# Optimization experiments

Measured on AMD Instinct MI355X. Metric: run time of the kernel, lower is better.

Reference implementation:

```python
import jax, jax.numpy as jnp
from jax import lax
import numpy as np

B, T, N, HORIZON = 64, 12, 512, 12
IN_DIM = 1; OUT_DIM = 1; YCOV = 1
RNN = 64; MEM_NUM = 20; MEM_DIM = 64; EMB = 10; CHEB_K = 3
DEC_DIM = RNN + MEM_DIM  # 128


def _xavier(key, shape):
    fan_in, fan_out = shape[0], shape[-1]
    std = float(np.sqrt(2.0 / (fan_in + fan_out)))
    return jax.random.normal(key, shape, dtype=jnp.float32) * std


def _cheb_feats(A, x, batched):
    mm = (lambda a, v: jnp.einsum('bnm,bmc->bnc', a, v)) if batched else (lambda a, v: jnp.einsum('nm,bmc->bnc', a, v))
    gs = [x, mm(A, x)]
    for _ in range(CHEB_K - 2):
        gs.append(2.0 * mm(A, gs[-1]) - gs[-2])
    return jnp.concatenate(gs, axis=-1)


def _agcn(x, A, W, b, batched):
    return _cheb_feats(A, x, batched) @ W + b


def _cell(x, state, A, Wg, bg, Wu, bu, batched):
    # AGCRN GRU cell
    hid = state.shape[-1]
    inp = jnp.concatenate([x, state], axis=-1)
    z_r = jax.nn.sigmoid(_agcn(inp, A, Wg, bg, batched))
    z, r = z_r[..., :hid], z_r[..., hid:]
    cand = jnp.concatenate([x, z * state], axis=-1)
    hc = jnp.tanh(_agcn(cand, A, Wu, bu, batched))
    return r * state + (1.0 - r) * hc


def _encode(x, A, Wg, bg, Wu, bu):
    # x: [B,T,N,C] -> last hidden state [B,N,RNN]
    xt = jnp.swapaxes(x, 0, 1)  # [T,B,N,C]
    init = jnp.zeros((x.shape[0], x.shape[2], RNN), x.dtype)
    def step(state, xt_):
        h = _cell(xt_, state, A, Wg, bg, Wu, bu, batched=False)
        return h, None
    h_t, _ = lax.scan(step, init, xt)
    return h_t


def _query_memory(h_t, Memory, Wq):
    q = h_t @ Wq                                   # [B,N,mem_dim]
    att = jax.nn.softmax(q @ Memory.T, axis=-1)    # [B,N,mem_num]
    value = att @ Memory                           # [B,N,mem_dim]
    _, ind = lax.top_k(att, 2)
    pos = Memory[ind[..., 0]]                      # [B,N,mem_dim]
    return value, pos


def setup_inputs() -> dict:
    key = jax.random.key(0)
    ks = jax.random.split(key, 20)
    x = jax.random.normal(ks[0], (B, T, N, IN_DIM), dtype=jnp.float32)
    x_cov = jax.random.normal(ks[1], (B, T, N, 1), dtype=jnp.float32)
    x_his = jax.random.normal(ks[2], (B, T, N, IN_DIM), dtype=jnp.float32)
    y_cov = jax.random.normal(ks[3], (B, HORIZON, N, YCOV), dtype=jnp.float32)
    a = jax.random.uniform(ks[4], (N, N), dtype=jnp.float32)
    adj = a / jnp.sum(a, axis=-1, keepdims=True)
    enc_in = IN_DIM + RNN
    dec_in = OUT_DIM + YCOV + DEC_DIM
    return {
        'x': x, 'x_cov': x_cov, 'x_his': x_his, 'y_cov': y_cov, 'adj': adj,
        'enc_gate_W': _xavier(ks[5], (CHEB_K * enc_in, 2 * RNN)),
        'enc_gate_b': jnp.zeros((2 * RNN,), jnp.float32),
        'enc_upd_W': _xavier(ks[6], (CHEB_K * enc_in, RNN)),
        'enc_upd_b': jnp.zeros((RNN,), jnp.float32),
        'dec_gate_W': _xavier(ks[7], (CHEB_K * dec_in, 2 * DEC_DIM)),
        'dec_gate_b': jnp.zeros((2 * DEC_DIM,), jnp.float32),
        'dec_upd_W': _xavier(ks[8], (CHEB_K * dec_in, DEC_DIM)),
        'dec_upd_b': jnp.zeros((DEC_DIM,), jnp.float32),
        'Memory': _xavier(ks[9], (MEM_NUM, MEM_DIM)),
        'Wq': _xavier(ks[10], (RNN, MEM_DIM)),
        'hyper_W': _xavier(ks[11], (DEC_DIM, EMB)),
        'hyper_b': jnp.zeros((EMB,), jnp.float32),
        'lat_W': _xavier(ks[12], (MEM_DIM, 1)),
        'lat_b': jnp.zeros((1,), jnp.float32),
        'proj_W': _xavier(ks[13], (DEC_DIM, OUT_DIM)),
        'proj_b': jnp.zeros((OUT_DIM,), jnp.float32),
    }


def reference(x, x_cov, x_his, y_cov, adj,
              enc_gate_W, enc_gate_b, enc_upd_W, enc_upd_b,
              dec_gate_W, dec_gate_b, dec_upd_W, dec_upd_b,
              Memory, Wq, hyper_W, hyper_b, lat_W, lat_b, proj_W, proj_b):
    # --- encoder on x and x_his (shared weights, single static support) ---
    h_t = _encode(x, adj, enc_gate_W, enc_gate_b, enc_upd_W, enc_upd_b)
    h_att, pos = _query_memory(h_t, Memory, Wq)
    h_his_t = _encode(x_his, adj, enc_gate_W, enc_gate_b, enc_upd_W, enc_upd_b)
    _, pos_his = _query_memory(h_his_t, Memory, Wq)
    # schema==1 latent distance head (sigmoid activation)
    latent_dis = jax.nn.sigmoid(((pos - pos_his) @ lat_W + lat_b)[..., 0])  # [B,N]
    # --- adaptive decoder support from hypernetwork ---
    h_aug = jnp.concatenate([h_t, h_att], axis=-1)          # [B,N,DEC_DIM]
    node_emb = h_aug @ hyper_W + hyper_b                    # [B,N,EMB]
    support = jax.nn.softmax(jax.nn.relu(jnp.einsum('bnc,bmc->bnm', node_emb, node_emb)), axis=-1)  # [B,N,N]
    # --- decoder rollout (inference path, no teacher forcing) ---
    go0 = jnp.zeros((x.shape[0], N, OUT_DIM), x.dtype)
    ycov_t = jnp.swapaxes(y_cov, 0, 1)  # [HORIZON,B,N,YCOV]
    def dec_step(carry, yc):
        go, h = carry
        xt = jnp.concatenate([go, yc], axis=-1)
        h = _cell(xt, h, support, dec_gate_W, dec_gate_b, dec_upd_W, dec_upd_b, batched=True)
        go = h @ proj_W + proj_b
        return (go, h), go
    _, outs = lax.scan(dec_step, (go0, h_aug), ycov_t)
    output = jnp.swapaxes(outs, 0, 1)  # [B,HORIZON,N,OUT_DIM]
    return output, latent_dis
```

## Files before the change

kernel.cpp:

```cpp
#include <hip/hip_runtime.h>
#include <hip/hip_bf16.h>


typedef __attribute__((ext_vector_type(8))) short s8v;
typedef __attribute__((ext_vector_type(4))) float f4v;
typedef __attribute__((ext_vector_type(4))) unsigned short u4v;

__device__ __forceinline__ float b2f(unsigned short u){
  union{unsigned int i; float f;} v; v.i = ((unsigned int)u)<<16; return v.f;
}
__device__ __forceinline__ unsigned short f2b(float f){
  union{float f; unsigned int i;} v; v.f = f;
  unsigned int r = v.i + 0x7fff + ((v.i >> 16) & 1);
  return (unsigned short)(r >> 16);
}

__global__ void k_zero16(uint4* p, int n){
  int i = blockIdx.x*256 + threadIdx.x;
  if (i < n) p[i] = make_uint4(0,0,0,0);
}


__global__ void k_reorderF(const float* __restrict__ W, float* __restrict__ Wr,
                           int HC, int NEX, int SEGW, int J){
  int idx = blockIdx.x*256 + threadIdx.x;
  int K = 3*SEGW;
  if (idx >= K*J) return;
  int k = idx / J, j = idx - k*J;
  int seg = k / SEGW, c = k - seg*SEGW;
  int CIN = HC + NEX;
  float v = 0.f;
  if (c < HC)       v = W[(size_t)(seg*CIN + NEX + c)*J + j];
  else if (c < CIN) v = W[(size_t)(seg*CIN + (c-HC))*J + j];
  Wr[(size_t)k*J + j] = v;
}

__global__ __launch_bounds__(256) void k_a2e(const float* __restrict__ A,
                                             float* __restrict__ A2e){
  __shared__ __align__(16) float As[32][132];
  __shared__ __align__(16) float Bs[32][132];
  int t = threadIdx.x;
  int r0 = (blockIdx.x & 3) * 128;
  int c0 = (blockIdx.x >> 2) * 128;
  int tr = t & 15, tc = t >> 4;
  float acc[8][8];
  #pragma unroll
  for (int i=0;i<8;i++)
    #pragma unroll
    for (int j=0;j<8;j++) acc[i][j]=0.f;
  for (int k0=0;k0<512;k0+=32){
    #pragma unroll
    for (int i=0;i<4;i++){
      int s = t + i*256;
      int k = s & 31, rq = s >> 5;
      const float* ap = A + (size_t)(r0 + rq*4)*512 + k0 + k;
      float4 v;
      v.x = ap[0]; v.y = ap[512]; v.z = ap[1024]; v.w = ap[1536];
      *(float4*)&As[k][rq*4] = v;
    }
    #pragma unroll
    for (int i=0;i<4;i++){
      int s = t + i*256;
      int k = s >> 5, cq = s & 31;
      float4 v = *(const float4*)(A + (size_t)(k0+k)*512 + c0 + cq*4);
      *(float4*)&Bs[k][cq*4] = v;
    }
    __syncthreads();
    #pragma unroll 8
    for (int k=0;k<32;k++){
      float a[8], b[8];
      *(float4*)&a[0] = *(const float4*)&As[k][tr*4];
      *(float4*)&a[4] = *(const float4*)&As[k][64+tr*4];
      *(float4*)&b[0] = *(const float4*)&Bs[k][tc*4];
      *(float4*)&b[4] = *(const float4*)&Bs[k][64+tc*4];
      #pragma unroll
      for (int i=0;i<8;i++)
        #pragma unroll
        for (int j=0;j<8;j++) acc[i][j] += a[i]*b[j];
    }
    __syncthreads();
  }
  #pragma unroll
  for (int i=0;i<8;i++){
    int r = r0 + (i<4 ? tr*4+i : 64+tr*4+i-4);
    #pragma unroll
    for (int j=0;j<8;j++){
      int c = c0 + (j<4 ? tc*4+j : 64+tc*4+j-4);
      A2e[(size_t)r*512 + c] = 2.f*acc[i][j] - (r==c ? 1.f : 0.f);
    }
  }
}

__global__ __launch_bounds__(256) void k_mm2F(
    const float* __restrict__ A, const float* __restrict__ A2e,
    const float* __restrict__ hsrc,
    const float* __restrict__ xa, const float* __restrict__ xb,
    int tstep, float* __restrict__ feats)
{
  __shared__ __align__(16) float As[32][68];
  __shared__ __align__(16) float A2s[32][68];
  __shared__ __align__(16) float Bs0[32][68];
  __shared__ __align__(16) float Bs1[32][68];
  const int t = threadIdx.x;
  const int z = blockIdx.z;
  const int n0 = blockIdx.x * 64;
  const int tr = t & 15, tc = t >> 4;
  const int xrow = t & 63, xmat = (t >> 6) & 1, xbb = t >> 7;
  const float* xp0 = xa + ((size_t)z*12 + tstep)*512;
  const float* xp1 = xb + ((size_t)z*12 + tstep)*512;
  float acc[2][2][4][4];
  #pragma unroll
  for (int m=0;m<2;m++)
    #pragma unroll
    for (int b=0;b<2;b++)
      #pragma unroll
      for (int i=0;i<4;i++)
        #pragma unroll
        for (int j=0;j<4;j++) acc[m][b][i][j]=0.f;
  float xacc = 0.f;

  for (int k0=0;k0<512;k0+=32){
    #pragma unroll
    for (int i=0;i<2;i++){
      int s = t + i*256;
      int k = s & 31, rq = s >> 5;
      const float* ap  = A   + (size_t)(n0 + rq*4)*512 + k0 + k;
      const float* a2p = A2e + (size_t)(n0 + rq*4)*512 + k0 + k;
      float4 v, w;
      v.x = ap[0];  v.y = ap[512];  v.z = ap[1024];  v.w = ap[1536];
      w.x = a2p[0]; w.y = a2p[512]; w.z = a2p[1024]; w.w = a2p[1536];
      *(float4*)&As[k][rq*4]  = v;
      *(float4*)&A2s[k][rq*4] = w;
    }
    #pragma unroll
    for (int i=0;i<2;i++){
      int s = t + i*256;
      int k = s >> 4, cq = s & 15;
      *(float4*)&Bs0[k][cq*4] = *(const float4*)(hsrc + (size_t)(z*512 + k0 + k)*64 + cq*4);
      *(float4*)&Bs1[k][cq*4] = *(const float4*)(hsrc + (size_t)((z+64)*512 + k0 + k)*64 + cq*4);
    }
    if (t < 32)      Bs0[t][64]    = xp0[k0 + t];
    else if (t < 64) Bs1[t-32][64] = xp1[k0 + t - 32];
    __syncthreads();
    #pragma unroll 4
    for (int k=0;k<32;k++){
      float a1[4], a2[4], b0[4], b1[4];
      *(float4*)&a1[0] = *(const float4*)&As[k][tr*4];
      *(float4*)&a2[0] = *(const float4*)&A2s[k][tr*4];
      *(float4*)&b0[0] = *(const float4*)&Bs0[k][tc*4];
      *(float4*)&b1[0] = *(const float4*)&Bs1[k][tc*4];
      #pragma unroll
      for (int i=0;i<4;i++)
        #pragma unroll
        for (int j=0;j<4;j++){
          acc[0][0][i][j] += a1[i]*b0[j];
          acc[0][1][i][j] += a1[i]*b1[j];
          acc[1][0][i][j] += a2[i]*b0[j];
          acc[1][1][i][j] += a2[i]*b1[j];
        }
      float am = xmat ? A2s[k][xrow] : As[k][xrow];
      xacc += am * (xbb ? Bs1[k][64] : Bs0[k][64]);
    }
    if ((k0 >> 6) == (int)blockIdx.x){
      for (int s=t; s<1088; s+=256){
        int sb = (s >= 544) ? 1 : 0;
        int ss = s - sb*544;
        int kk = ss/17, q = ss - kk*17;
        int bb = z + sb*64;
        float4 v;
        if (q < 16) v = sb ? *(const float4*)&Bs1[kk][q*4] : *(const float4*)&Bs0[kk][q*4];
        else        v = make_float4(sb ? Bs1[kk][64] : Bs0[kk][64], 0.f, 0.f, 0.f);
        *(float4*)(feats + (size_t)(bb*512 + k0 + kk)*204 + q*4) = v;
      }
    }
    __syncthreads();
  }
  #pragma unroll
  for (int bbi=0;bbi<2;bbi++){
    const int bb = z + bbi*64;
    #pragma unroll
    for (int i=0;i<4;i++){
      int row = n0 + tr*4 + i;
      float* fr = feats + (size_t)(bb*512 + row)*204;
      float4 v;
      v.x=acc[0][bbi][i][0]; v.y=acc[0][bbi][i][1];
      v.z=acc[0][bbi][i][2]; v.w=acc[0][bbi][i][3];
      *(float4*)(fr + 68 + tc*4) = v;
      v.x=acc[1][bbi][i][0]; v.y=acc[1][bbi][i][1];
      v.z=acc[1][bbi][i][2]; v.w=acc[1][bbi][i][3];
      *(float4*)(fr + 136 + tc*4) = v;
    }
  }
  feats[(size_t)((z + xbb*64)*512 + n0 + xrow)*204 + (xmat ? 136 : 68) + 64] = xacc;
}

__global__ __launch_bounds__(256) void k_gwG(
    const float* __restrict__ feats, const float* __restrict__ Wr,
    const float* __restrict__ bias,
    const float* __restrict__ hbuf, float* __restrict__ zh, float* __restrict__ rbuf)
{
  __shared__ __align__(16) float As[17][132];
  __shared__ __align__(16) float Ws[17][132];
  const int t = threadIdx.x;
  const int row0 = blockIdx.x * 128;
  const int tr = t & 15, tc = t >> 4;
  float acc[2][2][4][4];
  #pragma unroll
  for (int rg=0;rg<2;rg++)
    #pragma unroll
    for (int cg=0;cg<2;cg++)
      #pragma unroll
      for (int i=0;i<4;i++)
        #pragma unroll
        for (int j=0;j<4;j++) acc[rg][cg][i][j]=0.f;
  for (int kc=0; kc<204; kc+=17){
    for (int s=t; s<2176; s+=256){
      int r = s/17, k = s - r*17;
      As[k][r] = feats[(size_t)(row0+r)*204 + kc + k];
    }
    for (int s=t; s<2176; s+=256){
      int k = s >> 7, j = s & 127;
      Ws[k][j] = Wr[(size_t)(kc+k)*128 + j];
    }
    __syncthreads();
    #pragma unroll
    for (int k=0;k<17;k++){
      float a[8], w[8];
      *(float4*)&a[0] = *(const float4*)&As[k][tr*4];
      *(float4*)&a[4] = *(const float4*)&As[k][64+tr*4];
      *(float4*)&w[0] = *(const float4*)&Ws[k][tc*4];
      *(float4*)&w[4] = *(const float4*)&Ws[k][64+tc*4];
      #pragma unroll
      for (int rg=0;rg<2;rg++)
        #pragma unroll
        for (int i=0;i<4;i++)
          #pragma unroll
          for (int cg=0;cg<2;cg++)
            #pragma unroll
            for (int j=0;j<4;j++)
              acc[rg][cg][i][j] += a[rg*4+i]*w[cg*4+j];
    }
    __syncthreads();
  }
  float bj0[4], bj1[4];
  #pragma unroll
  for (int j=0;j<4;j++){ bj0[j] = bias[tc*4+j]; bj1[j] = bias[64+tc*4+j]; }
  #pragma unroll
  for (int rg=0;rg<2;rg++){
    #pragma unroll
    for (int i=0;i<4;i++){
      int row = row0 + rg*64 + tr*4 + i;
      float4 h4 = *(const float4*)(hbuf + (size_t)row*64 + tc*4);
      float hv[4] = {h4.x,h4.y,h4.z,h4.w};
      float4 oz, orr;
      float z[4], rr[4];
      #pragma unroll
      for (int j=0;j<4;j++){
        z[j]  = 1.f/(1.f + __expf(-(acc[rg][0][i][j] + bj0[j])));
        rr[j] = 1.f/(1.f + __expf(-(acc[rg][1][i][j] + bj1[j])));
      }
      oz.x=z[0]*hv[0]; oz.y=z[1]*hv[1]; oz.z=z[2]*hv[2]; oz.w=z[3]*hv[3];
      orr.x=rr[0]; orr.y=rr[1]; orr.z=rr[2]; orr.w=rr[3];
      *(float4*)(zh   + (size_t)row*64 + tc*4) = oz;
      *(float4*)(rbuf + (size_t)row*64 + tc*4) = orr;
    }
  }
}

__global__ __launch_bounds__(256) void k_gwU(
    const float* __restrict__ feats, const float* __restrict__ Wr,
    const float* __restrict__ bias,
    float* __restrict__ henc, const float* __restrict__ rbuf)
{
  __shared__ __align__(16) float As[17][132];
  __shared__ __align__(16) float Ws[17][68];
  const int t = threadIdx.x;
  const int row0 = blockIdx.x * 128;
  const int tr = t & 15, tc = t >> 4;
  float acc[2][4][4];
  #pragma unroll
  for (int rg=0;rg<2;rg++)
    #pragma unroll
    for (int i=0;i<4;i++)
      #pragma unroll
      for (int j=0;j<4;j++) acc[rg][i][j]=0.f;
  for (int kc=0; kc<204; kc+=17){
    for (int s=t; s<2176; s+=256){
      int r = s/17, k = s - r*17;
      As[k][r] = feats[(size_t)(row0+r)*204 + kc + k];
    }
    for (int s=t; s<1088; s+=256){
      int k = s >> 6, j = s & 63;
      Ws[k][j] = Wr[(size_t)(kc+k)*64 + j];
    }
    __syncthreads();
    #pragma unroll
    for (int k=0;k<17;k++){
      float a[8], w[4];
      *(float4*)&a[0] = *(const float4*)&As[k][tr*4];
      *(float4*)&a[4] = *(const float4*)&As[k][64+tr*4];
      *(float4*)&w[0] = *(const float4*)&Ws[k][tc*4];
      #pragma unroll
      for (int rg=0;rg<2;rg++)
        #pragma unroll
        for (int i=0;i<4;i++)
          #pragma unroll
          for (int j=0;j<4;j++)
            acc[rg][i][j] += a[rg*4+i]*w[j];
    }
    __syncthreads();
  }
  float bj[4];
  #pragma unroll
  for (int j=0;j<4;j++) bj[j] = bias[tc*4+j];
  #pragma unroll
  for (int rg=0;rg<2;rg++){
    #pragma unroll
    for (int i=0;i<4;i++){
      int row = row0 + rg*64 + tr*4 + i;
      float4 h4 = *(const float4*)(henc + (size_t)row*64 + tc*4);
      float4 r4 = *(const float4*)(rbuf + (size_t)row*64 + tc*4);
      float hv[4] = {h4.x,h4.y,h4.z,h4.w};
      float rv[4] = {r4.x,r4.y,r4.z,r4.w};
      float ov[4];
      #pragma unroll
      for (int j=0;j<4;j++){
        float hc = 1.f - 2.f/(__expf(2.f*(acc[rg][i][j] + bj[j])) + 1.f);
        ov[j] = rv[j]*hv[j] + (1.f - rv[j])*hc;
      }
      float4 o; o.x=ov[0]; o.y=ov[1]; o.z=ov[2]; o.w=ov[3];
      *(float4*)(henc + (size_t)row*64 + tc*4) = o;
    }
  }
}


__global__ void k_reorderB(const float* __restrict__ W, unsigned short* __restrict__ Wr,
                           int HC, int NEX, int C, int KP, int J){
  int idx = blockIdx.x*256 + threadIdx.x;
  if (idx >= J*KP) return;
  int j = idx / KP, kp = idx - j*KP;
  float v = 0.f;
  if (kp < 3*C){
    int seg = kp / C, c = kp - seg*C;
    int CIN = HC + NEX;
    if (c < HC)       v = W[(size_t)(seg*CIN + NEX + c)*J + j];
    else if (c < CIN) v = W[(size_t)(seg*CIN + (c-HC))*J + j];
  }
  Wr[(size_t)j*KP + kp] = f2b(v);
}

template<int C16, bool BETA>
__global__ __launch_bounds__(256) void k_mmB(
    const unsigned short* __restrict__ M, long long mstride,
    unsigned short* fC, int C3, int xseg, int oseg,
    unsigned short* fR, int KP, float alpha)
{
  constexpr int C = C16*16;
  constexpr int BIT = (C*4 + 255)/256;
  __shared__ unsigned short Bs[C*40];
  const int t = threadIdx.x;
  const int w = t >> 6, L = t & 63, lm = L & 15, q = L >> 4;
  const int bb = blockIdx.z;
  const int n0 = blockIdx.x * 128;
  const unsigned short* Mb = M + (size_t)bb * mstride;
  unsigned short* fCb = fC + (size_t)bb * C3 * 512;
  const unsigned short* Xb = fCb + (size_t)xseg * C * 512;
  const unsigned short* Yb = fCb;
  unsigned short* Ob = fCb + (size_t)oseg * C * 512;
  const int rw = n0 + w*32;

  f4v acc[2][C16];
  #pragma unroll
  for (int i=0;i<2;i++)
    #pragma unroll
    for (int j=0;j<C16;j++)
      #pragma unroll
      for (int r=0;r<4;r++) acc[i][j][r] = 0.f;

  s8v breg[BIT];
  const size_t ar0 = (size_t)(rw + lm)*512 + q*8;
  const size_t ar1 = (size_t)(rw + 16 + lm)*512 + q*8;

  #pragma unroll
  for (int i=0;i<BIT;i++){
    int s = t + i*256;
    if (s < C*4) breg[i] = *(const s8v*)(Xb + (size_t)(s>>2)*512 + (s&3)*8);
  }
  s8v a0 = *(const s8v*)(Mb + ar0);
  s8v a1 = *(const s8v*)(Mb + ar1);

  for (int ks=0; ks<16; ks++){
    #pragma unroll
    for (int i=0;i<BIT;i++){
      int s = t + i*256;
      if (s < C*4) *(s8v*)&Bs[(s>>2)*40 + (s&3)*8] = breg[i];
    }
    __syncthreads();
    const int kn = (ks < 15) ? (ks+1)*32 : 0;
    #pragma unroll
    for (int i=0;i<BIT;i++){
      int s = t + i*256;
      if (s < C*4) breg[i] = *(const s8v*)(Xb + (size_t)(s>>2)*512 + kn + (s&3)*8);
    }
    s8v a0n = *(const s8v*)(Mb + ar0 + kn);
    s8v a1n = *(const s8v*)(Mb + ar1 + kn);
    #pragma unroll
    for (int ct=0; ct<C16; ct++){
      s8v b = *(const s8v*)&Bs[(ct*16+lm)*40 + q*8];
      acc[0][ct] = __builtin_amdgcn_mfma_f32_16x16x32_bf16(a0, b, acc[0][ct], 0,0,0);
      acc[1][ct] = __builtin_amdgcn_mfma_f32_16x16x32_bf16(a1, b, acc[1][ct], 0,0,0);
    }
    __syncthreads();
    a0 = a0n; a1 = a1n;
  }
  #pragma unroll
  for (int rt=0; rt<2; rt++){
    const int m0 = rw + rt*16 + q*4;
    #pragma unroll
    for (int ct=0; ct<C16; ct++){
      const int c = ct*16 + lm;
      u4v o;
      if (BETA){
        u4v y = *(const u4v*)(Yb + (size_t)c*512 + m0);
        #pragma unroll
        for (int r=0;r<4;r++) o[r] = f2b(alpha*acc[rt][ct][r] - b2f(y[r]));
      } else {
        #pragma unroll
        for (int r=0;r<4;r++) o[r] = f2b(acc[rt][ct][r]);
      }
      *(u4v*)(Ob + (size_t)c*512 + m0) = o;
      const size_t rbase = (size_t)(bb*512 + m0)*KP + oseg*C + c;
      #pragma unroll
      for (int r=0;r<4;r++) fR[rbase + (size_t)r*KP] = o[r];
    }
  }
}

template<int KSTEPS, int JT16, int MODE, int HC>
__global__ __launch_bounds__(256) void k_gwB(
    unsigned short* fR, int KP,
    const unsigned short* __restrict__ Wr, const float* __restrict__ bias,
    unsigned short* fC, int C3,
    float* hC, float* rbuf)
{
  constexpr int JT = JT16*16;
  constexpr int BIT = JT*4/256;
  __shared__ unsigned short Bs[JT*40];
  const int t = threadIdx.x;
  const int w = t >> 6, L = t & 63, lm = L & 15, q = L >> 4;
  const int row0 = blockIdx.x * 128;
  const int j0 = blockIdx.y * JT;
  const int rw = row0 + w*32;

  f4v acc[2][JT16];
  #pragma unroll
  for (int i=0;i<2;i++)
    #pragma unroll
    for (int j=0;j<JT16;j++)
      #pragma unroll
      for (int r=0;r<4;r++) acc[i][j][r] = 0.f;

  s8v breg[BIT];
  const unsigned short* Wb = Wr + (size_t)j0*KP;
  const size_t ar0 = (size_t)(rw + lm)*KP + q*8;
  const size_t ar1 = (size_t)(rw + 16 + lm)*KP + q*8;

  #pragma unroll
  for (int i=0;i<BIT;i++){
    int s = t + i*256;
    breg[i] = *(const s8v*)(Wb + (size_t)(s>>2)*KP + (s&3)*8);
  }
  s8v a0 = *(const s8v*)(fR + ar0);
  s8v a1 = *(const s8v*)(fR + ar1);

  for (int ks=0; ks<KSTEPS; ks++){
    #pragma unroll
    for (int i=0;i<BIT;i++){
      int s = t + i*256;
      *(s8v*)&Bs[(s>>2)*40 + (s&3)*8] = breg[i];
    }
    __syncthreads();
    const int kn = (ks < KSTEPS-1) ? (ks+1)*32 : 0;
    #pragma unroll
    for (int i=0;i<BIT;i++){
      int s = t + i*256;
      breg[i] = *(const s8v*)(Wb + (size_t)(s>>2)*KP + kn + (s&3)*8);
    }
    s8v a0n = *(const s8v*)(fR + ar0 + kn);
    s8v a1n = *(const s8v*)(fR + ar1 + kn);
    #pragma unroll
    for (int ct=0; ct<JT16; ct++){
      s8v b = *(const s8v*)&Bs[(ct*16+lm)*40 + q*8];
      acc[0][ct] = __builtin_amdgcn_mfma_f32_16x16x32_bf16(a0, b, acc[0][ct], 0,0,0);
      acc[1][ct] = __builtin_amdgcn_mfma_f32_16x16x32_bf16(a1, b, acc[1][ct], 0,0,0);
    }
    __syncthreads();
    a0 = a0n; a1 = a1n;
  }
  #pragma unroll
  for (int rt=0; rt<2; rt++){
    const int m0 = rw + rt*16 + q*4;
    const int bb = m0 >> 9, n = m0 & 511;
    #pragma unroll
    for (int ct=0; ct<JT16; ct++){
      const int j = j0 + ct*16 + lm;
      const float bj = bias[j];
      if (MODE == 0){
        if (j < HC){
          f4v h4 = *(const f4v*)(hC + ((size_t)bb*HC + j)*512 + n);
          u4v o;
          #pragma unroll
          for (int r=0;r<4;r++){
            float s = 1.f/(1.f + __expf(-(acc[rt][ct][r] + bj)));
            float zh = s * h4[r];
            o[r] = f2b(zh);
            fR[(size_t)(m0+r)*KP + j] = o[r];
          }
          *(u4v*)(fC + ((size_t)bb*C3 + j)*512 + n) = o;
        } else {
          f4v rv;
          #pragma unroll
          for (int r=0;r<4;r++) rv[r] = 1.f/(1.f + __expf(-(acc[rt][ct][r] + bj)));
          *(f4v*)(rbuf + ((size_t)bb*HC + (j-HC))*512 + n) = rv;
        }
      } else {
        f4v h4 = *(const f4v*)(hC + ((size_t)bb*HC + j)*512 + n);
        f4v r4 = *(const f4v*)(rbuf + ((size_t)bb*HC + j)*512 + n);
        u4v o; f4v hn;
        #pragma unroll
        for (int r=0;r<4;r++){
          float e = __expf(2.f*(acc[rt][ct][r] + bj));
          float hc_ = 1.f - 2.f/(e + 1.f);
          hn[r] = r4[r]*h4[r] + (1.f - r4[r])*hc_;
          o[r] = f2b(hn[r]);
          fR[(size_t)(m0+r)*KP + j] = o[r];
        }
        *(f4v*)(hC + ((size_t)bb*HC + j)*512 + n) = hn;
        *(u4v*)(fC + ((size_t)bb*C3 + j)*512 + n) = o;
      }
    }
  }
}


__global__ void k_extras_dec(const float* __restrict__ yc,
    unsigned short* fR, unsigned short* fC, int tstep){
  int rr = blockIdx.x*256 + threadIdx.x;
  int bb = rr >> 9, n = rr & 511;
  unsigned short u = f2b(yc[((size_t)bb*12 + tstep)*512 + n]);
  fR[(size_t)rr*448 + 129] = u;
  fC[((size_t)bb*432 + 129)*512 + n] = u;
}
__global__ void k_fix_go(unsigned short* fR, unsigned short* fC){
  int rr = blockIdx.x*256 + threadIdx.x;
  int bb = rr >> 9, n = rr & 511;
  fR[(size_t)rr*448 + 128] = 0;
  fC[((size_t)bb*432 + 128)*512 + n] = 0;
}

__global__ __launch_bounds__(256) void k_query(const float* __restrict__ hR,
      const float* __restrict__ Wq, const float* __restrict__ Mem,
      float* __restrict__ hCd, unsigned short* fR, unsigned short* fC,
      int* __restrict__ it, int* __restrict__ ih){
  int sub = threadIdx.x >> 6, lane = threadIdx.x & 63;
  int row = blockIdx.x*4 + sub;
  __shared__ float sh[4][64], sq[4][64], ss[4][20];
  float hv = hR[(size_t)row*64 + lane];
  sh[sub][lane] = hv;
  __syncthreads();
  float qv = 0.f;
  for (int c=0;c<64;c++) qv += sh[sub][c]*Wq[c*64 + lane];
  sq[sub][lane] = qv;
  __syncthreads();
  if (lane < 20){
    float s = 0.f;
    for (int j=0;j<64;j++) s += sq[sub][j]*Mem[lane*64 + j];
    ss[sub][lane] = s;
  }
  __syncthreads();
  float mx = -1e30f; int am = 0;
  for (int m=0;m<20;m++){ float s = ss[sub][m]; if (s > mx){ mx = s; am = m; } }
  float sum = 0.f;
  for (int m=0;m<20;m++) sum += __expf(ss[sub][m]-mx);
  float inv = 1.f/sum;
  float v = 0.f;
  for (int m=0;m<20;m++) v += __expf(ss[sub][m]-mx)*inv*Mem[m*64 + lane];
  int bb = row >> 9, n = row & 511;
  if (bb < 64){
    hCd[((size_t)bb*128 + lane)*512 + n] = hv;
    hCd[((size_t)bb*128 + 64 + lane)*512 + n] = v;
    fR[(size_t)row*448 + lane] = f2b(hv);
    fR[(size_t)row*448 + 64 + lane] = f2b(v);
    fC[((size_t)bb*432 + lane)*512 + n] = f2b(hv);
    fC[((size_t)bb*432 + 64 + lane)*512 + n] = f2b(v);
    if (lane==0) it[row] = am;
  } else {
    if (lane==0) ih[row - 32768] = am;
  }
}

__global__ void k_latent(const int* __restrict__ it, const int* __restrict__ ih,
                         const float* __restrict__ Mem,
                         const float* __restrict__ lW, const float* __restrict__ lb,
                         float* __restrict__ outl){
  int row = blockIdx.x*256 + threadIdx.x;
  int i1 = it[row], i2 = ih[row];
  float a = lb[0];
  for (int c=0;c<64;c++) a += (Mem[i1*64+c]-Mem[i2*64+c])*lW[c];
  outl[row] = 1.f/(1.f + __expf(-a));
}

__global__ __launch_bounds__(256) void k_emb(const float* __restrict__ hCd,
    const float* __restrict__ hW, const float* __restrict__ hb, float* __restrict__ emb){
  __shared__ float sW[1280];
  int t = threadIdx.x;
  for (int s=t; s<1280; s+=256) sW[s] = hW[s];
  __syncthreads();
  int rr = blockIdx.x*256 + t;
  int bb = rr >> 9, n = rr & 511;
  float a[10];
  #pragma unroll
  for (int e=0;e<10;e++) a[e] = hb[e];
  for (int c=0;c<128;c++){
    float v = hCd[((size_t)bb*128 + c)*512 + n];
    #pragma unroll
    for (int e=0;e<10;e++) a[e] += v*sW[c*10+e];
  }
  #pragma unroll
  for (int e=0;e<10;e++) emb[(size_t)rr*10 + e] = a[e];
}

__global__ __launch_bounds__(256) void k_support(const float* __restrict__ emb,
                                                 unsigned short* __restrict__ sup){
  int b = blockIdx.x >> 9;
  int n = blockIdx.x & 511;
  int t = threadIdx.x;
  __shared__ float se[5120];
  __shared__ float red[8];
  for (int s = t; s < 5120; s += 256) se[s] = emb[(size_t)b*5120 + s];
  __syncthreads();
  float en[10];
  #pragma unroll
  for (int i=0;i<10;i++) en[i] = se[n*10+i];
  float s0=0.f, s1=0.f;
  #pragma unroll
  for (int i=0;i<10;i++){ s0 += en[i]*se[t*10+i]; s1 += en[i]*se[(t+256)*10+i]; }
  s0 = fmaxf(s0, 0.f); s1 = fmaxf(s1, 0.f);
  float mx = fmaxf(s0, s1);
  for (int o=32;o>0;o>>=1) mx = fmaxf(mx, __shfl_down(mx, o));
  if ((t&63)==0) red[t>>6] = mx;
  __syncthreads();
  mx = fmaxf(fmaxf(red[0],red[1]), fmaxf(red[2],red[3]));
  float e0 = __expf(s0-mx), e1 = __expf(s1-mx);
  float sm = e0 + e1;
  for (int o=32;o>0;o>>=1) sm += __shfl_down(sm, o);
  if ((t&63)==0) red[4+(t>>6)] = sm;
  __syncthreads();
  sm = red[4]+red[5]+red[6]+red[7];
  float inv = 1.f/sm;
  size_t base = ((size_t)b*512 + n)*512;
  sup[base + t]       = f2b(e0*inv);
  sup[base + t + 256] = f2b(e1*inv);
}

__global__ __launch_bounds__(256) void k_proj(const float* __restrict__ hCd,
    const float* __restrict__ pW, const float* __restrict__ pb,
    unsigned short* fR, unsigned short* fC, float* __restrict__ out, int tstep){
  __shared__ float sW[128];
  int t = threadIdx.x;
  if (t < 128) sW[t] = pW[t];
  __syncthreads();
  int rr = blockIdx.x*256 + t;
  int bb = rr >> 9, n = rr & 511;
  float a = pb[0];
  for (int c=0;c<128;c++) a += hCd[((size_t)bb*128 + c)*512 + n]*sW[c];
  out[((size_t)bb*12 + tstep)*512 + n] = a;
  unsigned short u = f2b(a);
  fR[(size_t)rr*448 + 128] = u;
  fC[((size_t)bb*432 + 128)*512 + n] = u;
}

extern "C" void kernel_launch(void* const* d_in, const int* in_sizes, int n_in,
                              void* d_out, int out_size, void* d_ws, size_t ws_size,
                              hipStream_t stream) {
  const float* x     = (const float*)d_in[0];
  const float* x_his = (const float*)d_in[2];
  const float* y_cov = (const float*)d_in[3];
  const float* adj   = (const float*)d_in[4];
  const float* egW   = (const float*)d_in[5];
  const float* egb   = (const float*)d_in[6];
  const float* euW   = (const float*)d_in[7];
  const float* eub   = (const float*)d_in[8];
  const float* dgW   = (const float*)d_in[9];
  const float* dgb   = (const float*)d_in[10];
  const float* duW   = (const float*)d_in[11];
  const float* dub   = (const float*)d_in[12];
  const float* Mem   = (const float*)d_in[13];
  const float* Wq    = (const float*)d_in[14];
  const float* hW    = (const float*)d_in[15];
  const float* hb    = (const float*)d_in[16];
  const float* lW    = (const float*)d_in[17];
  const float* lb    = (const float*)d_in[18];
  const float* pW    = (const float*)d_in[19];
  const float* pb    = (const float*)d_in[20];
  float* out  = (float*)d_out;
  float* outl = out + 393216;

  char* base = (char*)d_ws;
  size_t off = 0;
  auto alloc = [&](size_t bytes)->char*{
    char* p = base + off; off = (off + bytes + 255) & ~(size_t)255; return p;
  };
  float* featsF = (float*)alloc(53477376);
  unsigned short* sup = (unsigned short*)featsF;
  float* emb = featsF + 8650752;
  int*   it  = (int*)(featsF + 9961472);
  int*   ih  = it + 32768;
  float* henc = (float*)alloc(16777216);
  float* zhF  = (float*)alloc(16777216);
  float* hCd  = zhF;
  float* rbF  = (float*)alloc(16777216);
  unsigned short* fR = (unsigned short*)alloc(29360128);
  unsigned short* fC = (unsigned short*)alloc(28311552);
  float* a2e = (float*)alloc(1048576);
  float* wr_egF = (float*)alloc(104448);
  float* wr_euF = (float*)alloc(52224);
  unsigned short* wr_dg = (unsigned short*)alloc(229376);
  unsigned short* wr_du = (unsigned short*)alloc(114688);
  if (ws_size < off) return;

  k_zero16<<<4096,256,0,stream>>>((uint4*)henc, 1048576);
  k_zero16<<<7168,256,0,stream>>>((uint4*)fR, 1835008);
  k_zero16<<<6912,256,0,stream>>>((uint4*)fC, 1769472);
  k_a2e<<<16,256,0,stream>>>(adj, a2e);
  k_reorderF<<<102,256,0,stream>>>(egW, wr_egF, 64,1,68,128);
  k_reorderF<<< 51,256,0,stream>>>(euW, wr_euF, 64,1,68,64);
  k_reorderB<<<448,256,0,stream>>>(dgW, wr_dg, 128,2,144,448,256);
  k_reorderB<<<224,256,0,stream>>>(duW, wr_du, 128,2,144,448,128);

  for (int t = 0; t < 12; t++){
    k_mm2F<<<dim3(8,1,64),256,0,stream>>>(adj, a2e, henc, x, x_his, t, featsF);
    k_gwG<<<512,256,0,stream>>>(featsF, wr_egF, egb, henc, zhF, rbF);
    k_mm2F<<<dim3(8,1,64),256,0,stream>>>(adj, a2e, zhF, x, x_his, t, featsF);
    k_gwU<<<512,256,0,stream>>>(featsF, wr_euF, eub, henc, rbF);
  }

  k_query<<<16384,256,0,stream>>>(henc, Wq, Mem, hCd, fR, fC, it, ih);
  k_latent<<<128,256,0,stream>>>(it, ih, Mem, lW, lb, outl);
  k_emb<<<128,256,0,stream>>>(hCd, hW, hb, emb);
  k_support<<<32768,256,0,stream>>>(emb, sup);
  k_fix_go<<<128,256,0,stream>>>(fR, fC);

  for (int t = 0; t < 12; t++){
    k_extras_dec<<<128,256,0,stream>>>(y_cov, fR, fC, t);
    k_mmB<9,false><<<dim3(4,1,64),256,0,stream>>>(sup, 262144, fC, 432, 0, 1, fR, 448, 1.f);
    k_mmB<9,true ><<<dim3(4,1,64),256,0,stream>>>(sup, 262144, fC, 432, 1, 2, fR, 448, 2.f);
    k_gwB<14,16,0,128><<<dim3(256,1),256,0,stream>>>(fR, 448, wr_dg, dgb, fC, 432, hCd, rbF);
    k_mmB<9,false><<<dim3(4,1,64),256,0,stream>>>(sup, 262144, fC, 432, 0, 1, fR, 448, 1.f);
    k_mmB<9,true ><<<dim3(4,1,64),256,0,stream>>>(sup, 262144, fC, 432, 1, 2, fR, 448, 2.f);
    k_gwB<14,8,1,128><<<dim3(256,1),256,0,stream>>>(fR, 448, wr_du, dub, fC, 432, hCd, rbF);
    k_proj<<<128,256,0,stream>>>(hCd, pW, pb, fR, fC, out, t);
  }
}
```

Measured before the change: 7.304 ms.

## Fuse encoder graph-conv matmul with gate/update weight GEMM and epilogue

Merges the Chebyshev feature matmul kernel and the subsequent weight GEMM plus sigmoid/tanh GRU epilogue into a single templated encoder kernel. The features are kept in shared memory instead of being written to and re-read from a large global feats buffer. The grid is also reordered so batch is the fast axis. Weights are now read directly from global or cache inside the inner loop rather than staged in LDS. Shared memory per block grows, which may reduce occupancy.

Result: faster. 6.503 ms (-11.0%).

```diff
diff --git a/kernel.cpp b/kernel.cpp
--- a/kernel.cpp
+++ b/kernel.cpp
@@ -91,23 +91,32 @@
   }
 }
 
-__global__ __launch_bounds__(256) void k_mm2F(
+template<int MODE>
+__global__ __launch_bounds__(256) void k_enc(
     const float* __restrict__ A, const float* __restrict__ A2e,
     const float* __restrict__ hsrc,
     const float* __restrict__ xa, const float* __restrict__ xb,
-    int tstep, float* __restrict__ feats)
+    int tstep, const float* __restrict__ Wr, const float* __restrict__ bias,
+    float* __restrict__ zh, float* __restrict__ rbuf, float* __restrict__ henc)
 {
-  __shared__ __align__(16) float As[32][68];
-  __shared__ __align__(16) float A2s[32][68];
-  __shared__ __align__(16) float Bs0[32][68];
-  __shared__ __align__(16) float Bs1[32][68];
+  constexpr int J  = (MODE==0) ? 128 : 64;
+  constexpr int TN = (MODE==0) ? 8 : 4;
+  __shared__ __align__(16) float R1[8704];
+  __shared__ __align__(16) float F0t[2][65][66];
+  float (*sA)[68]   = (float(*)[68])(R1);
+  float (*sA2)[68]  = (float(*)[68])(R1 + 2176);
+  float (*sB0)[68]  = (float(*)[68])(R1 + 4352);
+  float (*sB1)[68]  = (float(*)[68])(R1 + 6528);
+  float (*G12s)[66] = (float(*)[66])(R1);
   const int t = threadIdx.x;
-  const int z = blockIdx.z;
-  const int n0 = blockIdx.x * 64;
+  const int z = blockIdx.x;
+  const int rowblk = blockIdx.z;
+  const int n0 = rowblk * 64;
   const int tr = t & 15, tc = t >> 4;
   const int xrow = t & 63, xmat = (t >> 6) & 1, xbb = t >> 7;
   const float* xp0 = xa + ((size_t)z*12 + tstep)*512;
   const float* xp1 = xb + ((size_t)z*12 + tstep)*512;
+
   float acc[2][2][4][4];
   #pragma unroll
   for (int m=0;m<2;m++)
@@ -129,26 +138,26 @@
       float4 v, w;
       v.x = ap[0];  v.y = ap[512];  v.z = ap[1024];  v.w = ap[1536];
       w.x = a2p[0]; w.y = a2p[512]; w.z = a2p[1024]; w.w = a2p[1536];
-      *(float4*)&As[k][rq*4]  = v;
-      *(float4*)&A2s[k][rq*4] = w;
+      *(float4*)&sA[k][rq*4]  = v;
+      *(float4*)&sA2[k][rq*4] = w;
     }
     #pragma unroll
     for (int i=0;i<2;i++){
       int s = t + i*256;
       int k = s >> 4, cq = s & 15;
-      *(float4*)&Bs0[k][cq*4] = *(const float4*)(hsrc + (size_t)(z*512 + k0 + k)*64 + cq*4);
-      *(float4*)&Bs1[k][cq*4] = *(const float4*)(hsrc + (size_t)((z+64)*512 + k0 + k)*64 + cq*4);
-    }
-    if (t < 32)      Bs0[t][64]    = xp0[k0 + t];
-    else if (t < 64) Bs1[t-32][64] = xp1[k0 + t - 32];
+      *(float4*)&sB0[k][cq*4] = *(const float4*)(hsrc + (size_t)(z*512 + k0 + k)*64 + cq*4);
+      *(float4*)&sB1[k][cq*4] = *(const float4*)(hsrc + (size_t)((z+64)*512 + k0 + k)*64 + cq*4);
+    }
+    if (t < 32)      sB0[t][64]    = xp0[k0 + t];
+    else if (t < 64) sB1[t-32][64] = xp1[k0 + t - 32];
     __syncthreads();
     #pragma unroll 4
     for (int k=0;k<32;k++){
       float a1[4], a2[4], b0[4], b1[4];
-      *(float4*)&a1[0] = *(const float4*)&As[k][tr*4];
-      *(float4*)&a2[0] = *(const float4*)&A2s[k][tr*4];
-      *(float4*)&b0[0] = *(const float4*)&Bs0[k][tc*4];
-      *(float4*)&b1[0] = *(const float4*)&Bs1[k][tc*4];
+      *(float4*)&a1[0] = *(const float4*)&sA[k][tr*4];
+      *(float4*)&a2[0] = *(const float4*)&sA2[k][tr*4];
+      *(float4*)&b0[0] = *(const float4*)&sB0[k][tc*4];
+      *(float4*)&b1[0] = *(const float4*)&sB1[k][tc*4];
       #pragma unroll
       for (int i=0;i<4;i++)
         #pragma unroll
@@ -158,179 +167,118 @@
           acc[1][0][i][j] += a2[i]*b0[j];
           acc[1][1][i][j] += a2[i]*b1[j];
         }
-      float am = xmat ? A2s[k][xrow] : As[k][xrow];
-      xacc += am * (xbb ? Bs1[k][64] : Bs0[k][64]);
-    }
-    if ((k0 >> 6) == (int)blockIdx.x){
-      for (int s=t; s<1088; s+=256){
-        int sb = (s >= 544) ? 1 : 0;
-        int ss = s - sb*544;
-        int kk = ss/17, q = ss - kk*17;
-        int bb = z + sb*64;
+      float am = xmat ? sA2[k][xrow] : sA[k][xrow];
+      xacc += am * (xbb ? sB1[k][64] : sB0[k][64]);
+    }
+    if ((k0 >> 6) == rowblk){
+      const int off = k0 & 63;
+      for (int s=t; s<4160; s+=256){
+        int sb = (s >= 2080) ? 1 : 0;
+        int ss = s - sb*2080;
+        int c = ss >> 5, kk = ss & 31;
+        F0t[sb][c][off + kk] = sb ? sB1[kk][c] : sB0[kk][c];
+      }
+    }
+    __syncthreads();
+  }
+
+  for (int bbi=0; bbi<2; bbi++){
+    #pragma unroll
+    for (int m=0;m<2;m++)
+      #pragma unroll
+      for (int j=0;j<4;j++){
         float4 v;
-        if (q < 16) v = sb ? *(const float4*)&Bs1[kk][q*4] : *(const float4*)&Bs0[kk][q*4];
-        else        v = make_float4(sb ? Bs1[kk][64] : Bs0[kk][64], 0.f, 0.f, 0.f);
-        *(float4*)(feats + (size_t)(bb*512 + k0 + kk)*204 + q*4) = v;
+        v.x = acc[m][bbi][0][j]; v.y = acc[m][bbi][1][j];
+        v.z = acc[m][bbi][2][j]; v.w = acc[m][bbi][3][j];
+        *(float4*)&G12s[m*65 + tc*4 + j][tr*4] = v;
       }
-    }
-    __syncthreads();
-  }
-  #pragma unroll
-  for (int bbi=0;bbi<2;bbi++){
-    const int bb = z + bbi*64;
+    if (xbb == bbi) G12s[xmat*65 + 64][xrow] = xacc;
+    __syncthreads();
+
+    float acc2[4][TN];
+    #pragma unroll
+    for (int i=0;i<4;i++)
+      #pragma unroll
+      for (int jj=0;jj<TN;jj++) acc2[i][jj]=0.f;
+    const int j0 = tc*TN;
+
+    #pragma unroll 4
+    for (int c=0;c<65;c++){
+      float a[4], w[TN];
+      *(float4*)&a[0] = *(const float4*)&F0t[bbi][c][tr*4];
+      #pragma unroll
+      for (int q=0;q<TN;q+=4) *(float4*)&w[q] = *(const float4*)(Wr + (size_t)c*J + j0 + q);
+      #pragma unroll
+      for (int i=0;i<4;i++)
+        #pragma unroll
+        for (int jj=0;jj<TN;jj++) acc2[i][jj] += a[i]*w[jj];
+    }
+    #pragma unroll 4
+    for (int c=0;c<65;c++){
+      float a[4], w[TN];
+      *(float4*)&a[0] = *(const float4*)&G12s[c][tr*4];
+      #pragma unroll
+      for (int q=0;q<TN;q+=4) *(float4*)&w[q] = *(const float4*)(Wr + (size_t)(68+c)*J + j0 + q);
+      #pragma unroll
+      for (int i=0;i<4;i++)
+        #pragma unroll
+        for (int jj=0;jj<TN;jj++) acc2[i][jj] += a[i]*w[jj];
+    }
+    #pragma unroll 4
+    for (int c=0;c<65;c++){
+      float a[4], w[TN];
+      *(float4*)&a[0] = *(const float4*)&G12s[65+c][tr*4];
+      #pragma unroll
+      for (int q=0;q<TN;q+=4) *(float4*)&w[q] = *(const float4*)(Wr + (size_t)(136+c)*J + j0 + q);
+      #pragma unroll
+      for (int i=0;i<4;i++)
+        #pragma unroll
+        for (int jj=0;jj<TN;jj++) acc2[i][jj] += a[i]*w[jj];
+    }
+
+    float bj[TN];
+    #pragma unroll
+    for (int jj=0;jj<TN;jj++) bj[jj] = bias[j0+jj];
+    const int gbase = (z + bbi*64)*512 + n0;
     #pragma unroll
     for (int i=0;i<4;i++){
-      int row = n0 + tr*4 + i;
-      float* fr = feats + (size_t)(bb*512 + row)*204;
-      float4 v;
-      v.x=acc[0][bbi][i][0]; v.y=acc[0][bbi][i][1];
-      v.z=acc[0][bbi][i][2]; v.w=acc[0][bbi][i][3];
-      *(float4*)(fr + 68 + tc*4) = v;
-      v.x=acc[1][bbi][i][0]; v.y=acc[1][bbi][i][1];
-      v.z=acc[1][bbi][i][2]; v.w=acc[1][bbi][i][3];
-      *(float4*)(fr + 136 + tc*4) = v;
-    }
-  }
-  feats[(size_t)((z + xbb*64)*512 + n0 + xrow)*204 + (xmat ? 136 : 68) + 64] = xacc;
-}
-
-__global__ __launch_bounds__(256) void k_gwG(
-    const float* __restrict__ feats, const float* __restrict__ Wr,
-    const float* __restrict__ bias,
-    const float* __restrict__ hbuf, float* __restrict__ zh, float* __restrict__ rbuf)
-{
-  __shared__ __align__(16) float As[17][132];
-  __shared__ __align__(16) float Ws[17][132];
-  const int t = threadIdx.x;
-  const int row0 = blockIdx.x * 128;
-  const int tr = t & 15, tc = t >> 4;
-  float acc[2][2][4][4];
-  #pragma unroll
-  for (int rg=0;rg<2;rg++)
-    #pragma unroll
-    for (int cg=0;cg<2;cg++)
-      #pragma unroll
-      for (int i=0;i<4;i++)
-        #pragma unroll
-        for (int j=0;j<4;j++) acc[rg][cg][i][j]=0.f;
-  for (int kc=0; kc<204; kc+=17){
-    for (int s=t; s<2176; s+=256){
-      int r = s/17, k = s - r*17;
-      As[k][r] = feats[(size_t)(row0+r)*204 + kc + k];
-    }
-    for (int s=t; s<2176; s+=256){
-      int k = s >> 7, j = s & 127;
-      Ws[k][j] = Wr[(size_t)(kc+k)*128 + j];
-    }
-    __syncthreads();
-    #pragma unroll
-    for (int k=0;k<17;k++){
-      float a[8], w[8];
-      *(float4*)&a[0] = *(const float4*)&As[k][tr*4];
-      *(float4*)&a[4] = *(const float4*)&As[k][64+tr*4];
-      *(float4*)&w[0] = *(const float4*)&Ws[k][tc*4];
-      *(float4*)&w[4] = *(const float4*)&Ws[k][64+tc*4];
-      #pragma unroll
-      for (int rg=0;rg<2;rg++)
-        #pragma unroll
-        for (int i=0;i<4;i++)
-          #pragma unroll
-          for (int cg=0;cg<2;cg++)
-            #pragma unroll
-            for (int j=0;j<4;j++)
-              acc[rg][cg][i][j] += a[rg*4+i]*w[cg*4+j];
-    }
-    __syncthreads();
-  }
-  float bj0[4], bj1[4];
-  #pragma unroll
-  for (int j=0;j<4;j++){ bj0[j] = bias[tc*4+j]; bj1[j] = bias[64+tc*4+j]; }
-  #pragma unroll
-  for (int rg=0;rg<2;rg++){
-    #pragma unroll
-    for (int i=0;i<4;i++){
-      int row = row0 + rg*64 + tr*4 + i;
-      float4 h4 = *(const float4*)(hbuf + (size_t)row*64 + tc*4);
-      float hv[4] = {h4.x,h4.y,h4.z,h4.w};
-      float4 oz, orr;
-      float z[4], rr[4];
-      #pragma unroll
-      for (int j=0;j<4;j++){
-        z[j]  = 1.f/(1.f + __expf(-(acc[rg][0][i][j] + bj0[j])));
-        rr[j] = 1.f/(1.f + __expf(-(acc[rg][1][i][j] + bj1[j])));
+      const int lr = tr*4 + i;
+      const int row = gbase + lr;
+      if (MODE == 0){
+        float s[8];
+        #pragma unroll
+        for (int jj=0;jj<TN;jj++) s[jj] = 1.f/(1.f + __expf(-(acc2[i][jj] + bj[jj])));
+        if (j0 < 64){
+          float4 o0, o1;
+          o0.x = s[0]*F0t[bbi][j0+0][lr]; o0.y = s[1]*F0t[bbi][j0+1][lr];
+          o0.z = s[2]*F0t[bbi][j0+2][lr]; o0.w = s[3]*F0t[bbi][j0+3][lr];
+          o1.x = s[4]*F0t[bbi][j0+4][lr]; o1.y = s[5]*F0t[bbi][j0+5][lr];
+          o1.z = s[6]*F0t[bbi][j0+6][lr]; o1.w = s[7]*F0t[bbi][j0+7][lr];
+          *(float4*)(zh + (size_t)row*64 + j0)     = o0;
+          *(float4*)(zh + (size_t)row*64 + j0 + 4) = o1;
+        } else {
+          float4 o0, o1;
+          o0.x=s[0]; o0.y=s[1]; o0.z=s[2]; o0.w=s[3];
+          o1.x=s[4]; o1.y=s[5]; o1.z=s[6]; o1.w=s[7];
+          *(float4*)(rbuf + (size_t)row*64 + j0 - 64) = o0;
+          *(float4*)(rbuf + (size_t)row*64 + j0 - 60) = o1;
+        }
+      } else {
+        float4 h4 = *(const float4*)(henc + (size_t)row*64 + j0);
+        float4 r4 = *(const float4*)(rbuf + (size_t)row*64 + j0);
+        float hv[4] = {h4.x,h4.y,h4.z,h4.w};
+        float rv[4] = {r4.x,r4.y,r4.z,r4.w};
+        float ov[4];
+        #pragma unroll
+        for (int jj=0;jj<4;jj++){
+          float hc = 1.f - 2.f/(__expf(2.f*(acc2[i][jj] + bj[jj])) + 1.f);
+          ov[jj] = rv[jj]*hv[jj] + (1.f - rv[jj])*hc;
+        }
+        float4 o; o.x=ov[0]; o.y=ov[1]; o.z=ov[2]; o.w=ov[3];
+        *(float4*)(henc + (size_t)row*64 + j0) = o;
       }
-      oz.x=z[0]*hv[0]; oz.y=z[1]*hv[1]; oz.z=z[2]*hv[2]; oz.w=z[3]*hv[3];
-      orr.x=rr[0]; orr.y=rr[1]; orr.z=rr[2]; orr.w=rr[3];
-      *(float4*)(zh   + (size_t)row*64 + tc*4) = oz;
-      *(float4*)(rbuf + (size_t)row*64 + tc*4) = orr;
-    }
-  }
-}
-
-__global__ __launch_bounds__(256) void k_gwU(
-    const float* __restrict__ feats, const float* __restrict__ Wr,
-    const float* __restrict__ bias,
-    float* __restrict__ henc, const float* __restrict__ rbuf)
-{
-  __shared__ __align__(16) float As[17][132];
-  __shared__ __align__(16) float Ws[17][68];
-  const int t = threadIdx.x;
-  const int row0 = blockIdx.x * 128;
-  const int tr = t & 15, tc = t >> 4;
-  float acc[2][4][4];
-  #pragma unroll
-  for (int rg=0;rg<2;rg++)
-    #pragma unroll
-    for (int i=0;i<4;i++)
-      #pragma unroll
-      for (int j=0;j<4;j++) acc[rg][i][j]=0.f;
-  for (int kc=0; kc<204; kc+=17){
-    for (int s=t; s<2176; s+=256){
-      int r = s/17, k = s - r*17;
-      As[k][r] = feats[(size_t)(row0+r)*204 + kc + k];
-    }
-    for (int s=t; s<1088; s+=256){
-      int k = s >> 6, j = s & 63;
-      Ws[k][j] = Wr[(size_t)(kc+k)*64 + j];
-    }
-    __syncthreads();
-    #pragma unroll
-    for (int k=0;k<17;k++){
-      float a[8], w[4];
-      *(float4*)&a[0] = *(const float4*)&As[k][tr*4];
-      *(float4*)&a[4] = *(const float4*)&As[k][64+tr*4];
-      *(float4*)&w[0] = *(const float4*)&Ws[k][tc*4];
-      #pragma unroll
-      for (int rg=0;rg<2;rg++)
-        #pragma unroll
-        for (int i=0;i<4;i++)
-          #pragma unroll
-          for (int j=0;j<4;j++)
-            acc[rg][i][j] += a[rg*4+i]*w[j];
-    }
-    __syncthreads();
-  }
-  float bj[4];
-  #pragma unroll
-  for (int j=0;j<4;j++) bj[j] = bias[tc*4+j];
-  #pragma unroll
-  for (int rg=0;rg<2;rg++){
-    #pragma unroll
-    for (int i=0;i<4;i++){
-      int row = row0 + rg*64 + tr*4 + i;
-      float4 h4 = *(const float4*)(henc + (size_t)row*64 + tc*4);
-      float4 r4 = *(const float4*)(rbuf + (size_t)row*64 + tc*4);
-      float hv[4] = {h4.x,h4.y,h4.z,h4.w};
-      float rv[4] = {r4.x,r4.y,r4.z,r4.w};
-      float ov[4];
-      #pragma unroll
-      for (int j=0;j<4;j++){
-        float hc = 1.f - 2.f/(__expf(2.f*(acc[rg][i][j] + bj[j])) + 1.f);
-        ov[j] = rv[j]*hv[j] + (1.f - rv[j])*hc;
-      }
-      float4 o; o.x=ov[0]; o.y=ov[1]; o.z=ov[2]; o.w=ov[3];
-      *(float4*)(henc + (size_t)row*64 + tc*4) = o;
-    }
+    }
+    __syncthreads();
   }
 }
 
@@ -712,10 +660,10 @@
   auto alloc = [&](size_t bytes)->char*{
     char* p = base + off; off = (off + bytes + 255) & ~(size_t)255; return p;
   };
-  float* featsF = (float*)alloc(53477376);
-  unsigned short* sup = (unsigned short*)featsF;
-  float* emb = featsF + 8650752;
-  int*   it  = (int*)(featsF + 9961472);
+  float* scratch = (float*)alloc(53477376);
+  unsigned short* sup = (unsigned short*)scratch;
+  float* emb = scratch + 8650752;
+  int*   it  = (int*)(scratch + 9961472);
   int*   ih  = it + 32768;
   float* henc = (float*)alloc(16777216);
   float* zhF  = (float*)alloc(16777216);
@@ -740,10 +688,10 @@
   k_reorderB<<<224,256,0,stream>>>(duW, wr_du, 128,2,144,448,128);
 
   for (int t = 0; t < 12; t++){
-    k_mm2F<<<dim3(8,1,64),256,0,stream>>>(adj, a2e, henc, x, x_his, t, featsF);
-    k_gwG<<<512,256,0,stream>>>(featsF, wr_egF, egb, henc, zhF, rbF);
-    k_mm2F<<<dim3(8,1,64),256,0,stream>>>(adj, a2e, zhF, x, x_his, t, featsF);
-    k_gwU<<<512,256,0,stream>>>(featsF, wr_euF, eub, henc, rbF);
+    k_enc<0><<<dim3(64,1,8),256,0,stream>>>(adj, a2e, henc, x, x_his, t,
+                                            wr_egF, egb, zhF, rbF, nullptr);
+    k_enc<1><<<dim3(64,1,8),256,0,stream>>>(adj, a2e, zhF, x, x_his, t,
+                                            wr_euF, eub, nullptr, rbF, henc);
   }
 
   k_query<<<16384,256,0,stream>>>(henc, Wq, Mem, hCd, fR, fC, it, ih);
```
